# Performance work log

Hardware: AMD Instinct MI355X
Metric: run time of the kernel (lower is better)

## Reference

```python
import jax, jax.numpy as jnp
import numpy as np

D_MODEL = 192; D_INNER = 384; N_STATE = 16; D_CONV = 4; DT_RANK = 12; DEPTH = 24
PATCH = 16; STRIDE = 16; IMG = 128; EPS = 1e-5


def _ln(x, w, b):
    m = jnp.mean(x, -1, keepdims=True)
    v = jnp.mean((x - m) ** 2, -1, keepdims=True)
    return (x - m) * jax.lax.rsqrt(v + EPS) * w + b


def _mamba_dir(xz, cw, cb, xpw, dpw, dpb, Alog, Dv):
    # xz: (B, L, 2*d_inner); one direction of the bidirectional Mamba mixer
    xp, z = jnp.split(xz, 2, axis=-1)               # (B,L,di) each
    xc = jnp.transpose(xp, (0, 2, 1))               # (B,di,L)
    xc = jnp.pad(xc, ((0, 0), (0, 0), (D_CONV - 1, 0)))  # causal pad
    xc = jax.lax.conv_general_dilated(
        xc, cw, (1,), 'VALID',
        dimension_numbers=('NCH', 'OIH', 'NCH'),
        feature_group_count=D_INNER) + cb[None, :, None]
    u = jax.nn.silu(jnp.transpose(xc, (0, 2, 1)))   # (B,L,di)
    dbl = u @ xpw.T                                  # (B,L,dt_rank+2N)
    dt, Bm, Cm = jnp.split(dbl, [DT_RANK, DT_RANK + N_STATE], axis=-1)
    dt = jax.nn.softplus(dt @ dpw.T + dpb)           # (B,L,di)
    A = -jnp.exp(Alog)                               # (di,N)
    dA = jnp.exp(dt[..., None] * A)                  # (B,L,di,N)
    dBu = (dt * u)[..., None] * Bm[:, :, None, :]    # (B,L,di,N)

    def comb(c1, c2):
        a1, b1 = c1
        a2, b2 = c2
        return a1 * a2, a2 * b1 + b2

    _, h = jax.lax.associative_scan(comb, (dA, dBu), axis=1)
    y = jnp.einsum('bldn,bln->bld', h, Cm) + u * Dv
    return y * jax.nn.silu(z)


def _forward(x, patch_w, patch_b, ln_w, ln_b, in_w,
             cf_w, cf_b, xpf_w, dtf_w, dtf_b, Alog_f, D_f,
             cbk_w, cbk_b, xpb_w, dtb_w, dtb_b, Alog_b, D_b,
             out_w, nf_w, nf_b, head_w, head_b):
    B = x.shape[0]
    p = jax.lax.conv_general_dilated(
        x, patch_w, (STRIDE,) * 3, 'VALID',
        dimension_numbers=('NCDHW', 'OIDHW', 'NCDHW')) + patch_b[None, :, None, None, None]
    hidden = p.reshape(B, D_MODEL, -1).transpose(0, 2, 1)  # (B, L=512, D)
    residual = jnp.zeros_like(hidden)

    xs = (ln_w, ln_b, in_w, cf_w, cf_b, xpf_w, dtf_w, dtf_b, Alog_f, D_f,
          cbk_w, cbk_b, xpb_w, dtb_w, dtb_b, Alog_b, D_b, out_w)

    def step(carry, pl):
        hidden, residual = carry
        (lw, lb, iw, cfw, cfb, xpf, dwf, dbf, Af, Dfv,
         cbw, cbb, xpb, dwb, dbb, Ab, Dbv, ow) = pl
        residual = residual + hidden
        hn = _ln(residual, lw, lb)
        xz = hn @ iw.T                               # (B,L,2di)
        yf = _mamba_dir(xz, cfw, cfb, xpf, dwf, dbf, Af, Dfv)
        yb = jnp.flip(_mamba_dir(jnp.flip(xz, 1), cbw, cbb, xpb, dwb, dbb, Ab, Dbv), 1)
        hidden = (yf + yb) @ ow.T
        return (hidden, residual), None

    (hidden, residual), _ = jax.lax.scan(step, (hidden, residual), xs)
    final = _ln(residual + hidden, nf_w, nf_b)
    feat = final[:, -1, :]                           # final_pool_type='none' -> last token
    return feat @ head_w.T + head_b


def setup_inputs() -> dict:
    key = jax.random.key(0)
    ks = jax.random.split(key, 16)
    rn = lambda k, s, sc=0.02: jax.random.normal(k, s, jnp.float32) * sc
    d = {}
    d['x'] = jax.random.normal(ks[0], (1, 1, IMG, IMG, IMG), jnp.float32)
    d['patch_w'] = rn(ks[1], (D_MODEL, 1, PATCH, PATCH, PATCH), 0.05)
    d['patch_b'] = jnp.zeros((D_MODEL,), jnp.float32)
    d['ln_w'] = jnp.ones((DEPTH, D_MODEL), jnp.float32)
    d['ln_b'] = jnp.zeros((DEPTH, D_MODEL), jnp.float32)
    d['in_w'] = rn(ks[2], (DEPTH, 2 * D_INNER, D_MODEL))
    d['cf_w'] = rn(ks[3], (DEPTH, D_INNER, 1, D_CONV), 0.2)
    d['cf_b'] = jnp.zeros((DEPTH, D_INNER), jnp.float32)
    d['xpf_w'] = rn(ks[4], (DEPTH, DT_RANK + 2 * N_STATE, D_INNER))
    d['dtf_w'] = rn(ks[5], (DEPTH, D_INNER, DT_RANK), 0.1)
    d['dtf_b'] = jnp.full((DEPTH, D_INNER), -4.6, jnp.float32)  # softplus -> dt~0.01
    d['Alog_f'] = jnp.log(jnp.broadcast_to(jnp.arange(1, N_STATE + 1, dtype=jnp.float32), (DEPTH, D_INNER, N_STATE)))
    d['D_f'] = jnp.ones((DEPTH, D_INNER), jnp.float32)
    d['cbk_w'] = rn(ks[6], (DEPTH, D_INNER, 1, D_CONV), 0.2)
    d['cbk_b'] = jnp.zeros((DEPTH, D_INNER), jnp.float32)
    d['xpb_w'] = rn(ks[7], (DEPTH, DT_RANK + 2 * N_STATE, D_INNER))
    d['dtb_w'] = rn(ks[8], (DEPTH, D_INNER, DT_RANK), 0.1)
    d['dtb_b'] = jnp.full((DEPTH, D_INNER), -4.6, jnp.float32)
    d['Alog_b'] = jnp.log(jnp.broadcast_to(jnp.arange(1, N_STATE + 1, dtype=jnp.float32), (DEPTH, D_INNER, N_STATE)))
    d['D_b'] = jnp.ones((DEPTH, D_INNER), jnp.float32)
    d['out_w'] = rn(ks[9], (DEPTH, D_MODEL, D_INNER))
    d['nf_w'] = jnp.ones((D_MODEL,), jnp.float32)
    d['nf_b'] = jnp.zeros((D_MODEL,), jnp.float32)
    d['head_w'] = rn(ks[10], (2, D_MODEL))
    d['head_b'] = jnp.zeros((2,), jnp.float32)
    return d


def reference(x, patch_w, patch_b, ln_w, ln_b, in_w,
              cf_w, cf_b, xpf_w, dtf_w, dtf_b, Alog_f, D_f,
              cbk_w, cbk_b, xpb_w, dtb_w, dtb_b, Alog_b, D_b,
              out_w, nf_w, nf_b, head_w, head_b):
    return _forward(x, patch_w, patch_b, ln_w, ln_b, in_w,
                    cf_w, cf_b, xpf_w, dtf_w, dtf_b, Alog_f, D_f,
                    cbk_w, cbk_b, xpb_w, dtb_w, dtb_b, Alog_b, D_b,
                    out_w, nf_w, nf_b, head_w, head_b)
```

## Files before the change

### kernel.cpp

```cpp
#include <hip/hip_runtime.h>
#include <hip/hip_bf16.h>

#define D_MODEL 192
#define D_INNER 384
#define N_STATE 16
#define DT_RANK 12
#define DEPTH 24
#define SEQ 512
#define NCHUNK 8
#define CLEN 64
#define TS 68
#define AS 33
#define PART_STRIDE (SEQ * D_MODEL)
#define USTR (SEQ * D_INNER)
#define KSPLIT 16
#define NBLK 512
#define FSTR 32
#define XZSTR (SEQ * 2 * D_INNER)
#define CHSTR (2 * NCHUNK * D_INNER * N_STATE)
#define GEN_OFF    512
#define SCANR_OFF  528
#define AFLAG_OFF  912
#define ABFLAG_OFF 1424
#define YFLAG_OFF  1936

typedef __hip_bfloat16 bf16;
typedef unsigned short u16;
typedef unsigned long long u64;

__device__ __forceinline__ float silu_f(float x) { return x / (1.f + __expf(-x)); }
__device__ __forceinline__ float softplus_f(float x) {
    return (x > 20.f) ? x : log1pf(__expf(x));
}
__device__ __forceinline__ float bf2f(unsigned u) {
    return __uint_as_float(u << 16);
}
__device__ __forceinline__ u16 f2bu(float f) {
    bf16 b = __float2bfloat16(f);
    return *reinterpret_cast<u16*>(&b);
}

__device__ __forceinline__ float aload(const float* p) {
    return __hip_atomic_load(p, __ATOMIC_RELAXED, __HIP_MEMORY_SCOPE_AGENT);
}
__device__ __forceinline__ void astore(float* p, float v) {
    __hip_atomic_store(p, v, __ATOMIC_RELAXED, __HIP_MEMORY_SCOPE_AGENT);
}
__device__ __forceinline__ unsigned aloadu(const unsigned* p) {
    return __hip_atomic_load(p, __ATOMIC_RELAXED, __HIP_MEMORY_SCOPE_AGENT);
}
__device__ __forceinline__ void astoreu(unsigned* p, unsigned v) {
    __hip_atomic_store(p, v, __ATOMIC_RELAXED, __HIP_MEMORY_SCOPE_AGENT);
}
__device__ __forceinline__ float2 aload2(const float* p) {
    const u64 v = __hip_atomic_load((const u64*)p, __ATOMIC_RELAXED, __HIP_MEMORY_SCOPE_AGENT);
    return make_float2(__uint_as_float((unsigned)v), __uint_as_float((unsigned)(v >> 32)));
}
__device__ __forceinline__ void astore2(float* p, float x, float y) {
    const u64 v = (u64)__float_as_uint(x) | ((u64)__float_as_uint(y) << 32);
    __hip_atomic_store((u64*)p, v, __ATOMIC_RELAXED, __HIP_MEMORY_SCOPE_AGENT);
}
__device__ __forceinline__ float4 aload4v(const float* p) {
    const float2 a = aload2(p), b = aload2(p + 2);
    return make_float4(a.x, a.y, b.x, b.y);
}
__device__ __forceinline__ float4 aload_bf4(const u16* p) {
    const u64 v = __hip_atomic_load((const u64*)p, __ATOMIC_RELAXED, __HIP_MEMORY_SCOPE_AGENT);
    return make_float4(bf2f((unsigned)(v & 0xffffu)),
                       bf2f((unsigned)((v >> 16) & 0xffffu)),
                       bf2f((unsigned)((v >> 32) & 0xffffu)),
                       bf2f((unsigned)(v >> 48)));
}
__device__ __forceinline__ void astore_bf4(u16* p, float a, float b, float c, float d) {
    const u64 v = (u64)f2bu(a) | ((u64)f2bu(b) << 16)
                | ((u64)f2bu(c) << 32) | ((u64)f2bu(d) << 48);
    __hip_atomic_store((u64*)p, v, __ATOMIC_RELAXED, __HIP_MEMORY_SCOPE_AGENT);
}

template<typename T> __device__ __forceinline__ float ld(const void* p, long i) {
    return ((const float*)p)[i];
}
template<> __device__ __forceinline__ float ld<bf16>(const void* p, long i) {
    return bf2f(((const u16*)p)[i]);
}
template<typename T> __device__ __forceinline__ float4 ld4(const void* p, long i) {
    return *(const float4*)((const float*)p + i);
}
template<> __device__ __forceinline__ float4 ld4<bf16>(const void* p, long i) {
    const ushort4 v = *(const ushort4*)((const u16*)p + i);
    return make_float4(bf2f(v.x), bf2f(v.y), bf2f(v.z), bf2f(v.w));
}
template<typename T> __device__ __forceinline__ void st(void* p, int i, float v) {
    ((float*)p)[i] = v;
}
template<> __device__ __forceinline__ void st<bf16>(void* p, int i, float v) {
    ((bf16*)p)[i] = __float2bfloat16(v);
}
__device__ __forceinline__ float dot4(const float4& a, const float4& b) {
    return a.x * b.x + a.y * b.y + a.z * b.z + a.w * b.w;
}
__device__ __forceinline__ void ld8b(const u16* p, float4& a, float4& b) {
    const uint4 u = *(const uint4*)p;
    a.x = bf2f(u.x & 0xffffu); a.y = bf2f(u.x >> 16);
    a.z = bf2f(u.y & 0xffffu); a.w = bf2f(u.y >> 16);
    b.x = bf2f(u.z & 0xffffu); b.y = bf2f(u.z >> 16);
    b.z = bf2f(u.w & 0xffffu); b.w = bf2f(u.w >> 16);
}
__device__ __forceinline__ float4 ld4b(const u16* p) {
    const uint2 u = *(const uint2*)p;
    return make_float4(bf2f(u.x & 0xffffu), bf2f(u.x >> 16),
                       bf2f(u.y & 0xffffu), bf2f(u.y >> 16));
}

__device__ __forceinline__ void post_flag(unsigned* fl, unsigned v, int tid) {
    asm volatile("s_waitcnt vmcnt(0)" ::: "memory");
    __syncthreads();
    if (tid == 0) astoreu(fl, v);
}
__device__ __forceinline__ void wait_flag(const unsigned* fl, unsigned v) {
    int spins = 0;
    while (aloadu(fl) < v) {
        if (++spins > (1 << 20)) break;
        __builtin_amdgcn_s_sleep(1);
    }
}

__device__ __forceinline__ void gbar(unsigned* bar, unsigned target, bool fence) {
    asm volatile("s_waitcnt vmcnt(0)" ::: "memory");
    __syncthreads();
    const int bid = blockIdx.x, tid = threadIdx.x;
    unsigned* gen0 = bar + GEN_OFF * FSTR;
    if (tid == 0) {
        if (fence) __threadfence();
        astoreu(&bar[bid * FSTR], target);
    }
    if (bid == 0) {
        int spins = 0;
        for (;;) {
            const unsigned va = aloadu(&bar[tid * FSTR]);
            const unsigned vb = aloadu(&bar[(tid + 256) * FSTR]);
            const bool ok = (va >= target) && (vb >= target);
            if (__syncthreads_and(ok)) break;
            if (++spins > (1 << 20)) break;
            __builtin_amdgcn_s_sleep(1);
        }
        if (tid == 0) astoreu(gen0, target);
    } else if (tid == 0) {
        int spins = 0;
        if (bid < 16) {
            while (aloadu(gen0) < target) {
                if (++spins > (1 << 20)) break;
                __builtin_amdgcn_s_sleep(2);
            }
            astoreu(&gen0[bid * FSTR], target);
        } else if (bid < 32) {
            while (aloadu(gen0) < target) {
                if (++spins > (1 << 20)) break;
                __builtin_amdgcn_s_sleep(2);
            }
        } else {
            unsigned* rl = &gen0[(bid >> 5) * FSTR];
            while (aloadu(rl) < target) {
                if (++spins > (1 << 20)) break;
                __builtin_amdgcn_s_sleep(2);
            }
        }
    }
    if (fence && tid == 0) __threadfence();
    __syncthreads();
}

__device__ void cvtB(const void* s, u16* d, long n, long g, long str, int isb) {
    if (isb) {
        const u16* p = (const u16*)s;
        for (long i = g * 4; i < n; i += str * 4) *(ushort4*)(d + i) = *(const ushort4*)(p + i);
    } else {
        const float* p = (const float*)s;
        for (long i = g * 4; i < n; i += str * 4) {
            const float4 v = *(const float4*)(p + i);
            ushort4 o; o.x = f2bu(v.x); o.y = f2bu(v.y); o.z = f2bu(v.z); o.w = f2bu(v.w);
            *(ushort4*)(d + i) = o;
        }
    }
}
__device__ void cvtF(const void* s, float* d, long n, long g, long str, int isb) {
    if (isb) {
        const u16* p = (const u16*)s;
        for (long i = g * 4; i < n; i += str * 4) {
            const ushort4 v = *(const ushort4*)(p + i);
            *(float4*)(d + i) = make_float4(bf2f(v.x), bf2f(v.y), bf2f(v.z), bf2f(v.w));
        }
    } else {
        const float* p = (const float*)s;
        for (long i = g * 4; i < n; i += str * 4) *(float4*)(d + i) = *(const float4*)(p + i);
    }
}
__device__ void cvtNA(const void* s, float* d, long n, long g, long str, int isb) {
    if (isb) {
        const u16* p = (const u16*)s;
        for (long i = g * 4; i < n; i += str * 4) {
            const ushort4 v = *(const ushort4*)(p + i);
            *(float4*)(d + i) = make_float4(-__expf(bf2f(v.x)), -__expf(bf2f(v.y)),
                                            -__expf(bf2f(v.z)), -__expf(bf2f(v.w)));
        }
    } else {
        const float* p = (const float*)s;
        for (long i = g * 4; i < n; i += str * 4) {
            const float4 v = *(const float4*)(p + i);
            *(float4*)(d + i) = make_float4(-__expf(v.x), -__expf(v.y), -__expf(v.z), -__expf(v.w));
        }
    }
}

template<typename T>
__device__ void final_phase(int tid, const float* res, const u16* yB, const void* ow,
                            const void* nw, const void* nb, const void* hw, const void* hb,
                            void* out, float* syf, float* f, float* red) {
    for (int j = tid; j < 96; j += 256) {
        const int q = j * 4;
        const float4 vf = aload_bf4(&yB[(long)511 * D_INNER + q]);
        const float4 vb = aload_bf4(&yB[(long)USTR + 511 * D_INNER + q]);
        *(float4*)&syf[q] = make_float4(vf.x + vb.x, vf.y + vb.y, vf.z + vb.z, vf.w + vb.w);
    }
    __syncthreads();
    float v = 0.f;
    if (tid < D_MODEL) {
        float acc = 0.f;
        const long wrow = (long)(DEPTH - 1) * D_MODEL * D_INNER + (long)tid * D_INNER;
        for (int k = 0; k < D_INNER; k += 4)
            acc += dot4(ld4<T>(ow, wrow + k), *(const float4*)&syf[k]);
        v = aload(&res[511 * D_MODEL + tid]) + acc;
    }
    float s = v;
    #pragma unroll
    for (int o = 32; o > 0; o >>= 1) s += __shfl_down(s, o, 64);
    if ((tid & 63) == 0 && tid < D_MODEL) red[tid >> 6] = s;
    __syncthreads();
    const float mean = (red[0] + red[1] + red[2]) * (1.f / D_MODEL);
    const float d = (tid < D_MODEL) ? (v - mean) : 0.f;
    float s2 = d * d;
    #pragma unroll
    for (int o = 32; o > 0; o >>= 1) s2 += __shfl_down(s2, o, 64);
    if ((tid & 63) == 0 && tid < D_MODEL) red[3 + (tid >> 6)] = s2;
    __syncthreads();
    const float var = (red[3] + red[4] + red[5]) * (1.f / D_MODEL);
    if (tid < D_MODEL)
        f[tid] = d * rsqrtf(var + 1e-5f) * ld<T>(nw, tid) + ld<T>(nb, tid);
    __syncthreads();
    if (tid < 2) {
        float a2 = ld<T>(hb, tid);
        for (int c = 0; c < D_MODEL; ++c) a2 += f[c] * ld<T>(hw, tid * D_MODEL + c);
        st<T>(out, tid, a2);
    }
}

struct MegaArgs {
    const void *x, *pw, *pb, *lnw, *lnb, *inw, *cfw, *cfb, *xpfw, *dtfw, *dtfb, *Af, *Dfv;
    const void *cbw, *cbb, *xpbw, *dtbw, *dtbb, *Ab, *Dbv, *ow, *nfw, *nfb, *hw, *hb;
    void* out;
    unsigned* bar;
    float *hidC, *res0, *res1, *dbl, *dt, *chunkH, *chunkP;
    u16 *xzB, *uB, *yB;
    float *lnwF, *lnbF, *cbfF, *cbbF, *dtbfF, *dtbbF, *negAfF, *negAbF, *DfF, *DbF, *pbF;
    u16 *inwB, *owB, *xB, *pwB, *xpwfB, *xpwbB, *dtwfB, *dtwbB, *cwfB, *cwbB;
};

__global__ void init_kernel(unsigned* bar) {
    const int i = blockIdx.x * 256 + threadIdx.x;
    ((uint4*)bar)[i] = make_uint4(0, 0, 0, 0);
}

__global__ void __launch_bounds__(256, 2) mega_kernel(MegaArgs a) {
    __shared__ float smem[6144];
    const int bid = blockIdx.x;
    const int tid = threadIdx.x;
    unsigned* bar = a.bar;
    unsigned* scanR  = a.bar + SCANR_OFF * FSTR;
    unsigned* aflag  = a.bar + AFLAG_OFF * FSTR;
    unsigned* abflag = a.bar + ABFLAG_OFF * FSTR;
    unsigned* yflag  = a.bar + YFLAG_OFF * FSTR;
    unsigned gen_ctr = 0;
    const int isb = (((const unsigned*)a.lnw)[0] != 0x3F800000u);

    {
        const long g = (long)bid * 256 + tid;
        const long str = (long)NBLK * 256;
        cvtB(a.inw,  a.inwB,  3538944, g, str, isb);
        cvtB(a.ow,   a.owB,   1769472, g, str, isb);
        cvtB(a.x,    a.xB,    2097152, g, str, isb);
        cvtB(a.pw,   a.pwB,    786432, g, str, isb);
        cvtB(a.xpfw, a.xpwfB,  405504, g, str, isb);
        cvtB(a.xpbw, a.xpwbB,  405504, g, str, isb);
        cvtB(a.dtfw, a.dtwfB,  110592, g, str, isb);
        cvtB(a.dtbw, a.dtwbB,  110592, g, str, isb);
        cvtB(a.cfw,  a.cwfB,    36864, g, str, isb);
        cvtB(a.cbw,  a.cwbB,    36864, g, str, isb);
        cvtF(a.lnw,  a.lnwF,     4608, g, str, isb);
        cvtF(a.lnb,  a.lnbF,     4608, g, str, isb);
        cvtF(a.cfb,  a.cbfF,     9216, g, str, isb);
        cvtF(a.cbb,  a.cbbF,     9216, g, str, isb);
        cvtF(a.dtfb, a.dtbfF,    9216, g, str, isb);
        cvtF(a.dtbb, a.dtbbF,    9216, g, str, isb);
        cvtF(a.pb,   a.pbF,       192, g, str, isb);
        cvtNA(a.Af,  a.negAfF,  147456, g, str, isb);
        cvtNA(a.Ab,  a.negAbF,  147456, g, str, isb);
        cvtF(a.Dfv,  a.DfF,      9216, g, str, isb);
        cvtF(a.Dbv,  a.DbF,      9216, g, str, isb);
    }
    gbar(bar, ++gen_ctr, true);

    {
        float* As_ = smem;
        float* Ws  = smem + 1056;
        const int ty = tid >> 4, tx = tid & 15;
        for (int unit = bid; unit < 768; unit += NBLK) {
            const int mt = unit & 15, nt = (unit >> 4) % 3, ks = unit / 48;
            const int m0 = mt * 32, n0 = nt * 64, kk0 = ks * 256;
            float acc[2][4] = {};
            for (int kk = kk0; kk < kk0 + 256; kk += 32) {
                for (int e = tid; e < 1024; e += 256) {
                    const int m = e >> 5, k = e & 31;
                    const int kid = kk + k, t = m0 + m;
                    const int dz = kid >> 8, dy = (kid >> 4) & 15, dx = kid & 15;
                    const int pz = t >> 6, py = (t >> 3) & 7, px = t & 7;
                    As_[k * AS + m] = bf2f(a.xB[(long)(pz * 16 + dz) * 16384 + (py * 16 + dy) * 128 + (px * 16 + dx)]);
                }
                for (int e = tid; e < 2048; e += 256) {
                    const int n = e >> 5, k = e & 31;
                    Ws[k * TS + n] = bf2f(a.pwB[(long)(n0 + n) * 4096 + kk + k]);
                }
                __syncthreads();
                #pragma unroll 8
                for (int k = 0; k < 32; ++k) {
                    const float a0 = As_[k * AS + ty * 2];
                    const float a1 = As_[k * AS + ty * 2 + 1];
                    const float4 w4 = *(const float4*)&Ws[k * TS + tx * 4];
                    acc[0][0] += a0 * w4.x; acc[0][1] += a0 * w4.y;
                    acc[0][2] += a0 * w4.z; acc[0][3] += a0 * w4.w;
                    acc[1][0] += a1 * w4.x; acc[1][1] += a1 * w4.y;
                    acc[1][2] += a1 * w4.z; acc[1][3] += a1 * w4.w;
                }
                __syncthreads();
            }
            float* C = a.hidC + (long)ks * PART_STRIDE;
            #pragma unroll
            for (int i = 0; i < 2; ++i) {
                float4 o4 = make_float4(acc[i][0], acc[i][1], acc[i][2], acc[i][3]);
                if (ks == 0) {
                    o4.x += a.pbF[n0 + tx * 4 + 0];
                    o4.y += a.pbF[n0 + tx * 4 + 1];
                    o4.z += a.pbF[n0 + tx * 4 + 2];
                    o4.w += a.pbF[n0 + tx * 4 + 3];
                }
                astore2(&C[(m0 + ty * 2 + i) * D_MODEL + n0 + tx * 4], o4.x, o4.y);
                astore2(&C[(m0 + ty * 2 + i) * D_MODEL + n0 + tx * 4 + 2], o4.z, o4.w);
            }
        }
    }
    gbar(bar, ++gen_ctr, false);

    const int ch = tid >> 4, np = tid & 15;
    float* sU  = smem;
    float* sDT = smem + 1024;
    float* sBC = smem + 2048;
    float* sZ  = smem + 4096;
    float* sY  = smem + 5120;

    for (int l = 0; l < DEPTH; ++l) {
        const int first = (l == 0);
        const unsigned lv = (unsigned)(l + 1);
        const int par = l & 1;
        u16* xzP = a.xzB + (long)par * XZSTR;
        u16* uP  = a.uB  + (long)par * (2 * USTR);
        float* dtP = a.dt + (long)par * (2 * USTR);
        float* dbG = a.dbl + (long)par * (2 * SEQ * 44);
        float* chH = a.chunkH + (long)par * CHSTR;
        float* chPb = a.chunkP + (long)par * CHSTR;
        const float* resIn = par ? a.res1 : a.res0;
        float* resOut      = par ? a.res0 : a.res1;

        {
            const int t = bid;
            if (par) {
                if (tid < 48) {
                    const int dd = tid / 24, dg = tid - dd * 24;
                    const int cf = t >> 6;
                    const int cbk = (511 - t) >> 6;
                    const int cc = dd ? cbk : cf;
                    wait_flag(&yflag[((dd * NCHUNK + cc) * 24 + dg) * FSTR], (unsigned)l);
                }
                __syncthreads();
            }
            float* sy  = smem;
            float* lnS = smem + 384;
            float* hnS = smem + 576;
            float* xzS = smem + 768;
            if (!first && tid < 96) {
                const int q4 = tid * 4;
                const long o = (long)t * D_INNER + q4;
                const float4 vf = aload_bf4(&a.yB[o]);
                const float4 vb = aload_bf4(&a.yB[(long)USTR + o]);
                *(float4*)&sy[q4] = make_float4(vf.x + vb.x, vf.y + vb.y, vf.z + vb.z, vf.w + vb.w);
            }
            __syncthreads();
            if (tid < D_MODEL) {
                float acc;
                if (first) {
                    float s = 0.f;
                    #pragma unroll
                    for (int sp = 0; sp < KSPLIT; ++sp)
                        s += aload(&a.hidC[(long)sp * PART_STRIDE + t * D_MODEL + tid]);
                    acc = s;
                } else {
                    acc = 0.f;
                    const u16* wr = a.owB + (long)(l - 1) * D_MODEL * D_INNER + (long)tid * D_INNER;
                    for (int k = 0; k < D_INNER; k += 8) {
                        float4 va, vb;
                        ld8b(wr + k, va, vb);
                        acc += dot4(va, *(const float4*)&sy[k]) + dot4(vb, *(const float4*)&sy[k + 4]);
                    }
                }
                const float rv = acc + (first ? 0.f : aload(&resIn[t * D_MODEL + tid]));
                lnS[tid] = rv;
                astore(&resOut[t * D_MODEL + tid], rv);
            }
            __syncthreads();
            {
                const int w = tid >> 6, lane = tid & 63;
                if (w == 0) {
                    const float v0 = lnS[lane];
                    const float v1 = lnS[lane + 64];
                    const float v2 = lnS[lane + 128];
                    float s = v0 + v1 + v2;
                    #pragma unroll
                    for (int o = 32; o > 0; o >>= 1) s += __shfl_xor(s, o, 64);
                    const float mean = s * (1.f / D_MODEL);
                    const float d0 = v0 - mean, d1 = v1 - mean, d2 = v2 - mean;
                    float s2 = d0 * d0 + d1 * d1 + d2 * d2;
                    #pragma unroll
                    for (int o = 32; o > 0; o >>= 1) s2 += __shfl_xor(s2, o, 64);
                    const float rstd = rsqrtf(s2 * (1.f / D_MODEL) + 1e-5f);
                    hnS[lane]       = d0 * rstd * a.lnwF[l * D_MODEL + lane]       + a.lnbF[l * D_MODEL + lane];
                    hnS[lane + 64]  = d1 * rstd * a.lnwF[l * D_MODEL + lane + 64]  + a.lnbF[l * D_MODEL + lane + 64];
                    hnS[lane + 128] = d2 * rstd * a.lnwF[l * D_MODEL + lane + 128] + a.lnbF[l * D_MODEL + lane + 128];
                }
            }
            __syncthreads();
            float accD[3] = {};
            const u16* w0 = a.inwB + (long)l * 2 * D_INNER * D_MODEL;
            for (int k = 0; k < D_MODEL; k += 8) {
                #pragma unroll
                for (int r = 0; r < 3; ++r) {
                    float4 va, vb;
                    ld8b(w0 + (long)(tid + r * 256) * D_MODEL + k, va, vb);
                    accD[r] += dot4(va, *(const float4*)&hnS[k])
                             + dot4(vb, *(const float4*)&hnS[k + 4]);
                }
            }
            #pragma unroll
            for (int r = 0; r < 3; ++r) xzS[tid + r * 256] = accD[r];
            __syncthreads();
            if (tid < 192) {
                const int q = tid * 4;
                const float* s = &xzS[q];
                astore_bf4(&xzP[(long)t * 2 * D_INNER + q], s[0], s[1], s[2], s[3]);
            }
            post_flag(&aflag[t * FSTR], lv, tid);

            if (tid < 7) {
                const int tt = t - 3 + tid;
                if (tt >= 0 && tt <= 511 && tt != t) wait_flag(&aflag[tt * FSTR], lv);
            }
            __syncthreads();

            float* su   = smem;
            float* dblP = smem + 1536;
            float* dblS = smem + 1712;
            if (tid < 192) {
                const int dirm = tid / 96, q4 = (tid - dirm * 96) * 4;
                const u16* cwB   = dirm ? a.cwbB  : a.cwfB;
                const float* cbF = dirm ? a.cbbF  : a.cbfF;
                float4 wA, wB2, wC, wD;
                ld8b(cwB + (long)(l * D_INNER + q4) * 4, wA, wB2);
                ld8b(cwB + (long)(l * D_INNER + q4) * 4 + 8, wC, wD);
                const float cw0[4] = {wA.x, wA.y, wA.z, wA.w};
                const float cw1[4] = {wB2.x, wB2.y, wB2.z, wB2.w};
                const float cw2[4] = {wC.x, wC.y, wC.z, wC.w};
                const float cw3[4] = {wD.x, wD.y, wD.z, wD.w};
                const int tok = dirm ? (511 - t) : t;
                float4 acc = *(const float4*)&cbF[l * D_INNER + q4];
                #pragma unroll
                for (int k = 0; k < 4; ++k) {
                    const int ii = tok + k - 3;
                    if (ii >= 0) {
                        const int src = dirm ? (511 - ii) : ii;
                        float4 xq;
                        if (src == t) xq = *(const float4*)&xzS[q4];
                        else          xq = aload_bf4(&xzP[(long)src * 2 * D_INNER + q4]);
                        acc.x += xq.x * cw0[k]; acc.y += xq.y * cw1[k];
                        acc.z += xq.z * cw2[k]; acc.w += xq.w * cw3[k];
                    }
                }
                const float u0 = silu_f(acc.x), u1 = silu_f(acc.y);
                const float u2 = silu_f(acc.z), u3 = silu_f(acc.w);
                *(float4*)&su[dirm * 384 + q4] = make_float4(u0, u1, u2, u3);
                astore_bf4(&uP[(long)dirm * USTR + (long)tok * D_INNER + q4], u0, u1, u2, u3);
            }
            __syncthreads();
            if (tid < 176) {
                const int dirm = tid / 88, r = tid - dirm * 88;
                const int half = r / 44, out = r - half * 44;
                const u16* xpwB = dirm ? a.xpwbB : a.xpwfB;
                const u16* wr = xpwB + (long)(l * 44 + out) * D_INNER;
                const int k0 = half * 192;
                float acc = 0.f;
                for (int k = k0; k < k0 + 192; k += 8) {
                    float4 va, vb;
                    ld8b(wr + k, va, vb);
                    acc += dot4(va, *(const float4*)&su[dirm * 384 + k])
                         + dot4(vb, *(const float4*)&su[dirm * 384 + k + 4]);
                }
                dblP[dirm * 88 + half * 44 + out] = acc;
            }
            __syncthreads();
            if (tid < 88) {
                const int dirm = tid / 44, out = tid - dirm * 44;
                const float s = dblP[dirm * 88 + out] + dblP[dirm * 88 + 44 + out];
                dblS[dirm * 44 + out] = s;
                const int tok = dirm ? (511 - t) : t;
                astore(&dbG[(long)dirm * SEQ * 44 + (long)tok * 44 + out], s);
            }
            __syncthreads();
            for (int j = tid; j < 384; j += 256) {
                const int dirm = j / 192, d2 = (j - dirm * 192) * 2;
                const u16* dtwB  = dirm ? a.dtwbB : a.dtwfB;
                const float* dtbF = dirm ? a.dtbbF : a.dtbfF;
                const int tok = dirm ? (511 - t) : t;
                const u16* wr = dtwB + (long)(l * D_INNER + d2) * DT_RANK;
                float4 A0, B0; ld8b(wr, A0, B0);
                const float4 C0 = ld4b(wr + 8);
                float4 A1, B1; ld8b(wr + 12, A1, B1);
                const float4 C1 = ld4b(wr + 20);
                const float4 ds0 = *(const float4*)&dblS[dirm * 44];
                const float4 ds1 = *(const float4*)&dblS[dirm * 44 + 4];
                const float4 ds2 = *(const float4*)&dblS[dirm * 44 + 8];
                const float acc0 = dtbF[l * D_INNER + d2]
                    + dot4(A0, ds0) + dot4(B0, ds1) + dot4(C0, ds2);
                const float acc1 = dtbF[l * D_INNER + d2 + 1]
                    + dot4(A1, ds0) + dot4(B1, ds1) + dot4(C1, ds2);
                astore2(&dtP[(long)dirm * USTR + (long)tok * D_INNER + d2],
                        softplus_f(acc0), softplus_f(acc1));
            }
            post_flag(&abflag[t * FSTR], lv, tid);
        }

        if (bid < 384) {
            const int dg = bid % 24, chunk = (bid / 24) & 7, dir2 = bid / 192;
            const int t0s = chunk * CLEN;
            if (tid < 64) {
                const int tg = t0s + tid;
                const int pb = dir2 ? (511 - tg) : tg;
                wait_flag(&abflag[pb * FSTR], lv);
            }
            __syncthreads();
            const int d0 = dg * 16, d = d0 + ch;
            const u16* ubq  = uP + (long)dir2 * USTR;
            const float* dtp = dtP + (long)dir2 * USTR;
            const float* db  = dbG + (long)dir2 * SEQ * 44;
            {
                const int t = tid >> 2, dl4 = (tid & 3) * 4;
                const int tg = t0s + t;
                const long base = (long)tg * D_INNER + d0 + dl4;
                *(float4*)&sU[t * 16 + dl4]  = aload_bf4(&ubq[base]);
                *(float4*)&sDT[t * 16 + dl4] = aload4v(&dtp[base]);
                const int out_l = dir2 ? (511 - tg) : tg;
                *(float4*)&sZ[t * 16 + dl4] = aload_bf4(&xzP[(long)out_l * 2 * D_INNER + D_INNER + d0 + dl4]);
            }
            for (int i = tid; i < 512; i += 256) {
                const int t = i >> 3, j4 = (i & 7) * 4;
                *(float4*)&sBC[t * 32 + j4] = aload4v(&db[(long)(t0s + t) * 44 + DT_RANK + j4]);
            }
            const float* negA = dir2 ? a.negAbF : a.negAfF;
            const float Areg = negA[(long)(l * D_INNER + d) * N_STATE + np];
            const float Dval = (dir2 ? a.DbF : a.DfF)[l * D_INNER + d];
            __syncthreads();
            float h = 0.f, dts = 0.f;
            for (int t = 0; t < CLEN; ++t) {
                const float dtv = sDT[t * 16 + ch];
                h = __expf(dtv * Areg) * h + (dtv * sU[t * 16 + ch]) * sBC[t * 32 + np];
                dts += dtv;
            }
            const long cb2 = ((long)(dir2 * NCHUNK + chunk) * D_INNER + d) * N_STATE + np;
            astore(&chH[cb2], h);
            astore(&chPb[cb2], __expf(Areg * dts));
            post_flag(&scanR[((dir2 * NCHUNK + chunk) * 24 + dg) * FSTR], lv, tid);
            if (tid < chunk) wait_flag(&scanR[((dir2 * NCHUNK + tid) * 24 + dg) * FSTR], lv);
            __syncthreads();
            float hs[NCHUNK - 1], ps[NCHUNK - 1];
            #pragma unroll
            for (int c = 0; c < NCHUNK - 1; ++c) {
                if (c < chunk) {
                    const long cbb = ((long)(dir2 * NCHUNK + c) * D_INNER + d) * N_STATE + np;
                    hs[c] = aload(&chH[cbb]);
                    ps[c] = aload(&chPb[cbb]);
                }
            }
            float h0 = 0.f;
            #pragma unroll
            for (int c = 0; c < NCHUNK - 1; ++c)
                if (c < chunk) h0 = ps[c] * h0 + hs[c];
            h = h0;
            for (int t = 0; t < CLEN; ++t) {
                const float dtv = sDT[t * 16 + ch];
                const float uv = sU[t * 16 + ch];
                h = __expf(dtv * Areg) * h + (dtv * uv) * sBC[t * 32 + np];
                float part = h * sBC[t * 32 + 16 + np];
                part += __shfl_xor(part, 1, 64);
                part += __shfl_xor(part, 2, 64);
                part += __shfl_xor(part, 4, 64);
                part += __shfl_xor(part, 8, 64);
                if (np == 0)
                    sY[t * 16 + ch] = (part + uv * Dval) * silu_f(sZ[t * 16 + ch]);
            }
            __syncthreads();
            {
                const int t = tid >> 2, dl4 = (tid & 3) * 4;
                const int tg = t0s + t;
                const int out_l = dir2 ? (511 - tg) : tg;
                u16* yb = a.yB + (long)dir2 * USTR;
                const float* s = &sY[t * 16 + dl4];
                astore_bf4(&yb[(long)out_l * D_INNER + d0 + dl4], s[0], s[1], s[2], s[3]);
            }
            post_flag(&yflag[((dir2 * NCHUNK + chunk) * 24 + dg) * FSTR], lv, tid);
        }
        if (par) gbar(bar, ++gen_ctr, false);
    }

    if (bid == 0) {
        float* syf = smem;
        float* f   = smem + 384;
        float* red = smem + 576;
        if (isb) final_phase<bf16>(tid, a.res0, a.yB, a.ow, a.nfw, a.nfb, a.hw, a.hb, a.out, syf, f, red);
        else     final_phase<float>(tid, a.res0, a.yB, a.ow, a.nfw, a.nfb, a.hw, a.hb, a.out, syf, f, red);
    }
}

extern "C" void kernel_launch(void* const* d_in, const int* in_sizes, int n_in,
                              void* d_out, int out_size, void* d_ws, size_t ws_size,
                              hipStream_t stream) {
    (void)in_sizes; (void)n_in; (void)out_size; (void)ws_size;
    const void* x    = d_in[0];
    const void* pw   = d_in[1];
    const void* pb   = d_in[2];
    const void* lnw  = d_in[3];
    const void* lnb  = d_in[4];
    const void* inw  = d_in[5];
    const void* cfw  = d_in[6];
    const void* cfb  = d_in[7];
    const void* xpfw = d_in[8];
    const void* dtfw = d_in[9];
    const void* dtfb = d_in[10];
    const void* Af   = d_in[11];
    const void* Dfv  = d_in[12];
    const void* cbw  = d_in[13];
    const void* cbb  = d_in[14];
    const void* xpbw = d_in[15];
    const void* dtbw = d_in[16];
    const void* dtbb = d_in[17];
    const void* Ab   = d_in[18];
    const void* Dbv  = d_in[19];
    const void* ow   = d_in[20];
    const void* nfw  = d_in[21];
    const void* nfb  = d_in[22];
    const void* hw   = d_in[23];
    const void* hb   = d_in[24];

    unsigned* bar = (unsigned*)d_ws;
    float* w = (float*)((char*)d_ws + 524288);
    float* hidC   = w;  w += KSPLIT * PART_STRIDE;
    float* res0   = w;  w += PART_STRIDE;
    float* res1   = w;  w += PART_STRIDE;
    float* dbl    = w;  w += 2 * 2 * SEQ * 44;
    float* dt     = w;  w += 2 * 2 * USTR;
    float* chunkH = w;  w += 2 * CHSTR;
    float* chunkP = w;  w += 2 * CHSTR;
    float* lnwF = w;  w += 4608;
    float* lnbF = w;  w += 4608;
    float* cbfF = w;  w += 9216;
    float* cbbF = w;  w += 9216;
    float* dtbfF = w; w += 9216;
    float* dtbbF = w; w += 9216;
    float* negAfF = w; w += 147456;
    float* negAbF = w; w += 147456;
    float* DfF = w;   w += 9216;
    float* DbF = w;   w += 9216;
    float* pbF = w;   w += 192;
    u16* b = (u16*)w;
    u16* xzB = b;  b += 2 * XZSTR;
    u16* uB  = b;  b += 2 * 2 * USTR;
    u16* yB  = b;  b += 2 * USTR;
    u16* inwB  = b;  b += 3538944;
    u16* owB   = b;  b += 1769472;
    u16* xB    = b;  b += 2097152;
    u16* pwB   = b;  b += 786432;
    u16* xpwfB = b;  b += 405504;
    u16* xpwbB = b;  b += 405504;
    u16* dtwfB = b;  b += 110592;
    u16* dtwbB = b;  b += 110592;
    u16* cwfB  = b;  b += 36864;
    u16* cwbB  = b;  b += 36864;

    MegaArgs ma;
    ma.x = x; ma.pw = pw; ma.pb = pb; ma.lnw = lnw; ma.lnb = lnb; ma.inw = inw;
    ma.cfw = cfw; ma.cfb = cfb; ma.xpfw = xpfw; ma.dtfw = dtfw; ma.dtfb = dtfb;
    ma.Af = Af; ma.Dfv = Dfv; ma.cbw = cbw; ma.cbb = cbb; ma.xpbw = xpbw;
    ma.dtbw = dtbw; ma.dtbb = dtbb; ma.Ab = Ab; ma.Dbv = Dbv; ma.ow = ow;
    ma.nfw = nfw; ma.nfb = nfb; ma.hw = hw; ma.hb = hb; ma.out = d_out;
    ma.bar = bar;
    ma.hidC = hidC; ma.res0 = res0; ma.res1 = res1; ma.dbl = dbl; ma.dt = dt;
    ma.chunkH = chunkH; ma.chunkP = chunkP;
    ma.xzB = xzB; ma.uB = uB; ma.yB = yB;
    ma.lnwF = lnwF; ma.lnbF = lnbF; ma.cbfF = cbfF; ma.cbbF = cbbF;
    ma.dtbfF = dtbfF; ma.dtbbF = dtbbF; ma.negAfF = negAfF; ma.negAbF = negAbF;
    ma.DfF = DfF; ma.DbF = DbF; ma.pbF = pbF;
    ma.inwB = inwB; ma.owB = owB; ma.xB = xB; ma.pwB = pwB;
    ma.xpwfB = xpwfB; ma.xpwbB = xpwbB; ma.dtwfB = dtwfB; ma.dtwbB = dtwbB;
    ma.cwfB = cwfB; ma.cwbB = cwbB;

    init_kernel<<<128, 256, 0, stream>>>(bar);
    mega_kernel<<<NBLK, 256, 0, stream>>>(ma);
}
```

Before: 1.802 ms.

## Double mega-kernel block size to 512 threads and split per-token GEMVs across them

Launches the persistent mega kernel with 512 threads per block instead of 256. The extra threads split the out-projection GEMV into two K halves reduced through shared memory, cover the in-projection rows without a per-thread loop, and take over the dt-projection and B/C staging loops. Phases built for 256 threads (patch conv, chunk scan) are now guarded so the upper half of the block idles there. This trades more register pressure under the new launch bounds and idle threads in some phases for more parallelism in the serial per-token stage. Shared-memory offsets are rearranged to fit the new partial buffers.

```diff
diff --git a/kernel.cpp b/kernel.cpp
--- a/kernel.cpp
+++ b/kernel.cpp
@@ -15,6 +15,7 @@
 #define USTR (SEQ * D_INNER)
 #define KSPLIT 16
 #define NBLK 512
+#define NTHR 512
 #define FSTR 32
 #define XZSTR (SEQ * 2 * D_INNER)
 #define CHSTR (2 * NCHUNK * D_INNER * N_STATE)
@@ -138,8 +139,7 @@
         int spins = 0;
         for (;;) {
             const unsigned va = aloadu(&bar[tid * FSTR]);
-            const unsigned vb = aloadu(&bar[(tid + 256) * FSTR]);
-            const bool ok = (va >= target) && (vb >= target);
+            const bool ok = (va >= target);
             if (__syncthreads_and(ok)) break;
             if (++spins > (1 << 20)) break;
             __builtin_amdgcn_s_sleep(1);
@@ -216,8 +216,8 @@
 __device__ void final_phase(int tid, const float* res, const u16* yB, const void* ow,
                             const void* nw, const void* nb, const void* hw, const void* hb,
                             void* out, float* syf, float* f, float* red) {
-    for (int j = tid; j < 96; j += 256) {
-        const int q = j * 4;
+    if (tid < 96) {
+        const int q = tid * 4;
         const float4 vf = aload_bf4(&yB[(long)511 * D_INNER + q]);
         const float4 vb = aload_bf4(&yB[(long)USTR + 511 * D_INNER + q]);
         *(float4*)&syf[q] = make_float4(vf.x + vb.x, vf.y + vb.y, vf.z + vb.z, vf.w + vb.w);
@@ -270,8 +270,8 @@
     ((uint4*)bar)[i] = make_uint4(0, 0, 0, 0);
 }
 
-__global__ void __launch_bounds__(256, 2) mega_kernel(MegaArgs a) {
-    __shared__ float smem[6144];
+__global__ void __launch_bounds__(NTHR, 4) mega_kernel(MegaArgs a) {
+    __shared__ float smem[6464];
     const int bid = blockIdx.x;
     const int tid = threadIdx.x;
     unsigned* bar = a.bar;
@@ -283,8 +283,8 @@
     const int isb = (((const unsigned*)a.lnw)[0] != 0x3F800000u);
 
     {
-        const long g = (long)bid * 256 + tid;
-        const long str = (long)NBLK * 256;
+        const long g = (long)bid * NTHR + tid;
+        const long str = (long)NBLK * NTHR;
         cvtB(a.inw,  a.inwB,  3538944, g, str, isb);
         cvtB(a.ow,   a.owB,   1769472, g, str, isb);
         cvtB(a.x,    a.xB,    2097152, g, str, isb);
@@ -318,42 +318,46 @@
             const int m0 = mt * 32, n0 = nt * 64, kk0 = ks * 256;
             float acc[2][4] = {};
             for (int kk = kk0; kk < kk0 + 256; kk += 32) {
-                for (int e = tid; e < 1024; e += 256) {
+                for (int e = tid; e < 1024; e += NTHR) {
                     const int m = e >> 5, k = e & 31;
                     const int kid = kk + k, t = m0 + m;
                     const int dz = kid >> 8, dy = (kid >> 4) & 15, dx = kid & 15;
                     const int pz = t >> 6, py = (t >> 3) & 7, px = t & 7;
                     As_[k * AS + m] = bf2f(a.xB[(long)(pz * 16 + dz) * 16384 + (py * 16 + dy) * 128 + (px * 16 + dx)]);
                 }
-                for (int e = tid; e < 2048; e += 256) {
+                for (int e = tid; e < 2048; e += NTHR) {
                     const int n = e >> 5, k = e & 31;
                     Ws[k * TS + n] = bf2f(a.pwB[(long)(n0 + n) * 4096 + kk + k]);
                 }
                 __syncthreads();
-                #pragma unroll 8
-                for (int k = 0; k < 32; ++k) {
-                    const float a0 = As_[k * AS + ty * 2];
-                    const float a1 = As_[k * AS + ty * 2 + 1];
-                    const float4 w4 = *(const float4*)&Ws[k * TS + tx * 4];
-                    acc[0][0] += a0 * w4.x; acc[0][1] += a0 * w4.y;
-                    acc[0][2] += a0 * w4.z; acc[0][3] += a0 * w4.w;
-                    acc[1][0] += a1 * w4.x; acc[1][1] += a1 * w4.y;
-                    acc[1][2] += a1 * w4.z; acc[1][3] += a1 * w4.w;
+                if (tid < 256) {
+                    #pragma unroll 8
+                    for (int k = 0; k < 32; ++k) {
+                        const float a0 = As_[k * AS + ty * 2];
+                        const float a1 = As_[k * AS + ty * 2 + 1];
+                        const float4 w4 = *(const float4*)&Ws[k * TS + tx * 4];
+                        acc[0][0] += a0 * w4.x; acc[0][1] += a0 * w4.y;
+                        acc[0][2] += a0 * w4.z; acc[0][3] += a0 * w4.w;
+                        acc[1][0] += a1 * w4.x; acc[1][1] += a1 * w4.y;
+                        acc[1][2] += a1 * w4.z; acc[1][3] += a1 * w4.w;
+                    }
                 }
                 __syncthreads();
             }
-            float* C = a.hidC + (long)ks * PART_STRIDE;
-            #pragma unroll
-            for (int i = 0; i < 2; ++i) {
-                float4 o4 = make_float4(acc[i][0], acc[i][1], acc[i][2], acc[i][3]);
-                if (ks == 0) {
-                    o4.x += a.pbF[n0 + tx * 4 + 0];
-                    o4.y += a.pbF[n0 + tx * 4 + 1];
-                    o4.z += a.pbF[n0 + tx * 4 + 2];
-                    o4.w += a.pbF[n0 + tx * 4 + 3];
-                }
-                astore2(&C[(m0 + ty * 2 + i) * D_MODEL + n0 + tx * 4], o4.x, o4.y);
-                astore2(&C[(m0 + ty * 2 + i) * D_MODEL + n0 + tx * 4 + 2], o4.z, o4.w);
+            if (tid < 256) {
+                float* C = a.hidC + (long)ks * PART_STRIDE;
+                #pragma unroll
+                for (int i = 0; i < 2; ++i) {
+                    float4 o4 = make_float4(acc[i][0], acc[i][1], acc[i][2], acc[i][3]);
+                    if (ks == 0) {
+                        o4.x += a.pbF[n0 + tx * 4 + 0];
+                        o4.y += a.pbF[n0 + tx * 4 + 1];
+                        o4.z += a.pbF[n0 + tx * 4 + 2];
+                        o4.w += a.pbF[n0 + tx * 4 + 3];
+                    }
+                    astore2(&C[(m0 + ty * 2 + i) * D_MODEL + n0 + tx * 4], o4.x, o4.y);
+                    astore2(&C[(m0 + ty * 2 + i) * D_MODEL + n0 + tx * 4 + 2], o4.z, o4.w);
+                }
             }
         }
     }
@@ -392,9 +396,10 @@
                 __syncthreads();
             }
             float* sy  = smem;
-            float* lnS = smem + 384;
-            float* hnS = smem + 576;
-            float* xzS = smem + 768;
+            float* lnP = smem + 384;
+            float* lnS = smem + 768;
+            float* hnS = smem + 960;
+            float* xzS = smem + 1152;
             if (!first && tid < 96) {
                 const int q4 = tid * 4;
                 const long o = (long)t * D_INNER + q4;
@@ -403,26 +408,35 @@
                 *(float4*)&sy[q4] = make_float4(vf.x + vb.x, vf.y + vb.y, vf.z + vb.z, vf.w + vb.w);
             }
             __syncthreads();
-            if (tid < D_MODEL) {
-                float acc;
-                if (first) {
+            if (first) {
+                if (tid < D_MODEL) {
                     float s = 0.f;
                     #pragma unroll
                     for (int sp = 0; sp < KSPLIT; ++sp)
                         s += aload(&a.hidC[(long)sp * PART_STRIDE + t * D_MODEL + tid]);
-                    acc = s;
-                } else {
-                    acc = 0.f;
-                    const u16* wr = a.owB + (long)(l - 1) * D_MODEL * D_INNER + (long)tid * D_INNER;
-                    for (int k = 0; k < D_INNER; k += 8) {
+                    lnS[tid] = s;
+                    astore(&resOut[t * D_MODEL + tid], s);
+                }
+            } else {
+                if (tid < 384) {
+                    const int row = tid % 192, kh = tid / 192;
+                    const u16* wr = a.owB + (long)(l - 1) * D_MODEL * D_INNER
+                                  + (long)row * D_INNER + kh * 192;
+                    const float* syh = &sy[kh * 192];
+                    float acc = 0.f;
+                    for (int k = 0; k < 192; k += 8) {
                         float4 va, vb;
                         ld8b(wr + k, va, vb);
-                        acc += dot4(va, *(const float4*)&sy[k]) + dot4(vb, *(const float4*)&sy[k + 4]);
+                        acc += dot4(va, *(const float4*)&syh[k]) + dot4(vb, *(const float4*)&syh[k + 4]);
                     }
-                }
-                const float rv = acc + (first ? 0.f : aload(&resIn[t * D_MODEL + tid]));
-                lnS[tid] = rv;
-                astore(&resOut[t * D_MODEL + tid], rv);
+                    lnP[kh * 192 + row] = acc;
+                }
+                __syncthreads();
+                if (tid < D_MODEL) {
+                    const float rv = lnP[tid] + lnP[192 + tid] + aload(&resIn[t * D_MODEL + tid]);
+                    lnS[tid] = rv;
+                    astore(&resOut[t * D_MODEL + tid], rv);
+                }
             }
             __syncthreads();
             {
@@ -446,19 +460,24 @@
                 }
             }
             __syncthreads();
-            float accD[3] = {};
-            const u16* w0 = a.inwB + (long)l * 2 * D_INNER * D_MODEL;
-            for (int k = 0; k < D_MODEL; k += 8) {
-                #pragma unroll
-                for (int r = 0; r < 3; ++r) {
+            {
+                const u16* w0 = a.inwB + (long)l * 2 * D_INNER * D_MODEL;
+                float accD0 = 0.f, accD1 = 0.f;
+                const u16* wr0 = w0 + (long)tid * D_MODEL;
+                const u16* wr1 = w0 + (long)(tid + 256) * D_MODEL;
+                for (int k = 0; k < D_MODEL; k += 8) {
                     float4 va, vb;
-                    ld8b(w0 + (long)(tid + r * 256) * D_MODEL + k, va, vb);
-                    accD[r] += dot4(va, *(const float4*)&hnS[k])
-                             + dot4(vb, *(const float4*)&hnS[k + 4]);
-                }
-            }
-            #pragma unroll
-            for (int r = 0; r < 3; ++r) xzS[tid + r * 256] = accD[r];
+                    ld8b(wr0 + k, va, vb);
+                    accD0 += dot4(va, *(const float4*)&hnS[k]) + dot4(vb, *(const float4*)&hnS[k + 4]);
+                    if (tid >= 256) {
+                        float4 vc, vd;
+                        ld8b(wr1 + k, vc, vd);
+                        accD1 += dot4(vc, *(const float4*)&hnS[k]) + dot4(vd, *(const float4*)&hnS[k + 4]);
+                    }
+                }
+                xzS[tid] = accD0;
+                if (tid >= 256) xzS[tid + 256] = accD1;
+            }
             __syncthreads();
             if (tid < 192) {
                 const int q = tid * 4;
@@ -473,9 +492,9 @@
             }
             __syncthreads();
 
-            float* su   = smem;
-            float* dblP = smem + 1536;
-            float* dblS = smem + 1712;
+            float* su   = smem + 1984;
+            float* dblP = smem + 2752;
+            float* dblS = smem + 2928;
             if (tid < 192) {
                 const int dirm = tid / 96, q4 = (tid - dirm * 96) * 4;
                 const u16* cwB   = dirm ? a.cwbB  : a.cwfB;
@@ -531,8 +550,8 @@
                 astore(&dbG[(long)dirm * SEQ * 44 + (long)tok * 44 + out], s);
             }
             __syncthreads();
-            for (int j = tid; j < 384; j += 256) {
-                const int dirm = j / 192, d2 = (j - dirm * 192) * 2;
+            if (tid < 384) {
+                const int dirm = tid / 192, d2 = (tid - dirm * 192) * 2;
                 const u16* dtwB  = dirm ? a.dtwbB : a.dtwfB;
                 const float* dtbF = dirm ? a.dtbbF : a.dtbfF;
                 const int tok = dirm ? (511 - t) : t;
@@ -567,7 +586,7 @@
             const u16* ubq  = uP + (long)dir2 * USTR;
             const float* dtp = dtP + (long)dir2 * USTR;
             const float* db  = dbG + (long)dir2 * SEQ * 44;
-            {
+            if (tid < 256) {
                 const int t = tid >> 2, dl4 = (tid & 3) * 4;
                 const int tg = t0s + t;
                 const long base = (long)tg * D_INNER + d0 + dl4;
@@ -576,54 +595,61 @@
                 const int out_l = dir2 ? (511 - tg) : tg;
                 *(float4*)&sZ[t * 16 + dl4] = aload_bf4(&xzP[(long)out_l * 2 * D_INNER + D_INNER + d0 + dl4]);
             }
-            for (int i = tid; i < 512; i += 256) {
-                const int t = i >> 3, j4 = (i & 7) * 4;
-                *(float4*)&sBC[t * 32 + j4] = aload4v(&db[(long)(t0s + t) * 44 + DT_RANK + j4]);
-            }
-            const float* negA = dir2 ? a.negAbF : a.negAfF;
-            const float Areg = negA[(long)(l * D_INNER + d) * N_STATE + np];
-            const float Dval = (dir2 ? a.DbF : a.DfF)[l * D_INNER + d];
-            __syncthreads();
-            float h = 0.f, dts = 0.f;
-            for (int t = 0; t < CLEN; ++t) {
-                const float dtv = sDT[t * 16 + ch];
-                h = __expf(dtv * Areg) * h + (dtv * sU[t * 16 + ch]) * sBC[t * 32 + np];
-                dts += dtv;
-            }
-            const long cb2 = ((long)(dir2 * NCHUNK + chunk) * D_INNER + d) * N_STATE + np;
-            astore(&chH[cb2], h);
-            astore(&chPb[cb2], __expf(Areg * dts));
+            {
+                const int i = tid;
+                const int tt = i >> 3, j4 = (i & 7) * 4;
+                *(float4*)&sBC[tt * 32 + j4] = aload4v(&db[(long)(t0s + tt) * 44 + DT_RANK + j4]);
+            }
+            float Areg = 0.f, Dval = 0.f;
+            if (tid < 256) {
+                const float* negA = dir2 ? a.negAbF : a.negAfF;
+                Areg = negA[(long)(l * D_INNER + d) * N_STATE + np];
+                Dval = (dir2 ? a.DbF : a.DfF)[l * D_INNER + d];
+            }
+            __syncthreads();
+            if (tid < 256) {
+                float h = 0.f, dts = 0.f;
+                for (int t = 0; t < CLEN; ++t) {
+                    const float dtv = sDT[t * 16 + ch];
+                    h = __expf(dtv * Areg) * h + (dtv * sU[t * 16 + ch]) * sBC[t * 32 + np];
+                    dts += dtv;
+                }
+                const long cb2 = ((long)(dir2 * NCHUNK + chunk) * D_INNER + d) * N_STATE + np;
+                astore(&chH[cb2], h);
+                astore(&chPb[cb2], __expf(Areg * dts));
+            }
             post_flag(&scanR[((dir2 * NCHUNK + chunk) * 24 + dg) * FSTR], lv, tid);
             if (tid < chunk) wait_flag(&scanR[((dir2 * NCHUNK + tid) * 24 + dg) * FSTR], lv);
             __syncthreads();
-            float hs[NCHUNK - 1], ps[NCHUNK - 1];
-            #pragma unroll
-            for (int c = 0; c < NCHUNK - 1; ++c) {
-                if (c < chunk) {
-                    const long cbb = ((long)(dir2 * NCHUNK + c) * D_INNER + d) * N_STATE + np;
-                    hs[c] = aload(&chH[cbb]);
-                    ps[c] = aload(&chPb[cbb]);
-                }
-            }
-            float h0 = 0.f;
-            #pragma unroll
-            for (int c = 0; c < NCHUNK - 1; ++c)
-                if (c < chunk) h0 = ps[c] * h0 + hs[c];
-            h = h0;
-            for (int t = 0; t < CLEN; ++t) {
-                const float dtv = sDT[t * 16 + ch];
-                const float uv = sU[t * 16 + ch];
-                h = __expf(dtv * Areg) * h + (dtv * uv) * sBC[t * 32 + np];
-                float part = h * sBC[t * 32 + 16 + np];
-                part += __shfl_xor(part, 1, 64);
-                part += __shfl_xor(part, 2, 64);
-                part += __shfl_xor(part, 4, 64);
-                part += __shfl_xor(part, 8, 64);
-                if (np == 0)
-                    sY[t * 16 + ch] = (part + uv * Dval) * silu_f(sZ[t * 16 + ch]);
-            }
-            __syncthreads();
-            {
+            if (tid < 256) {
+                float hs[NCHUNK - 1], ps[NCHUNK - 1];
+                #pragma unroll
+                for (int c = 0; c < NCHUNK - 1; ++c) {
+                    if (c < chunk) {
+                        const long cbb = ((long)(dir2 * NCHUNK + c) * D_INNER + d) * N_STATE + np;
+                        hs[c] = aload(&chH[cbb]);
+                        ps[c] = aload(&chPb[cbb]);
+                    }
+                }
+                float h = 0.f;
+                #pragma unroll
+                for (int c = 0; c < NCHUNK - 1; ++c)
+                    if (c < chunk) h = ps[c] * h + hs[c];
+                for (int t = 0; t < CLEN; ++t) {
+                    const float dtv = sDT[t * 16 + ch];
+                    const float uv = sU[t * 16 + ch];
+                    h = __expf(dtv * Areg) * h + (dtv * uv) * sBC[t * 32 + np];
+                    float part = h * sBC[t * 32 + 16 + np];
+                    part += __shfl_xor(part, 1, 64);
+                    part += __shfl_xor(part, 2, 64);
+                    part += __shfl_xor(part, 4, 64);
+                    part += __shfl_xor(part, 8, 64);
+                    if (np == 0)
+                        sY[t * 16 + ch] = (part + uv * Dval) * silu_f(sZ[t * 16 + ch]);
+                }
+            }
+            __syncthreads();
+            if (tid < 256) {
                 const int t = tid >> 2, dl4 = (tid & 3) * 4;
                 const int tg = t0s + t;
                 const int out_l = dir2 ? (511 - tg) : tg;
@@ -728,5 +754,5 @@
     ma.cwfB = cwfB; ma.cwbB = cwbB;
 
     init_kernel<<<128, 256, 0, stream>>>(bar);
-    mega_kernel<<<NBLK, 256, 0, stream>>>(ma);
-}
+    mega_kernel<<<NBLK, NTHR, 0, stream>>>(ma);
+}
```

Result: slower. 4.994 ms (+177.2%).
